# Optimization experiments

Measured on AMD Instinct MI355X. Metric: run time of the kernel, lower is better.

## Reference

```python
import jax, jax.numpy as jnp
import numpy as np

N_NODES = 100000
N_EDGES = 3200000
D_IN = 128
D_HID = 16
N_CLS = 2


def gcn_conv(x, edge_index, W, b, n_nodes):
    """PyG GCNConv (normalize=True, add_self_loops=True, bias=True)."""
    h = x @ W  # [N, out]
    loop = jnp.arange(n_nodes, dtype=edge_index.dtype)
    src = jnp.concatenate([edge_index[0], loop])
    dst = jnp.concatenate([edge_index[1], loop])
    deg = jax.ops.segment_sum(jnp.ones_like(dst, dtype=h.dtype), dst, num_segments=n_nodes)
    dinv = jnp.where(deg > 0, jax.lax.rsqrt(deg), jnp.zeros_like(deg))
    norm = dinv[src] * dinv[dst]  # [E+N]
    msg = h[src] * norm[:, None]  # gather + scale
    out = jax.ops.segment_sum(msg, dst, num_segments=n_nodes)  # scatter-add
    return out + b


def setup_inputs() -> dict:
    key = jax.random.key(0)
    k1, k2, k3, k4, k5 = jax.random.split(key, 5)
    x = jax.random.normal(k1, (N_NODES, D_IN), dtype=jnp.float32)
    edge_index = jax.random.randint(k2, (2, N_EDGES), 0, N_NODES, dtype=jnp.int64)
    # Glorot-style init for GCNConv weights, zeros for bias (PyG default)
    W1 = jax.random.normal(k3, (D_IN, D_HID), dtype=jnp.float32) * (1.0 / np.sqrt(D_IN))
    b1 = jnp.zeros((D_HID,), dtype=jnp.float32)
    W2 = jax.random.normal(k4, (D_HID, N_CLS), dtype=jnp.float32) * (1.0 / np.sqrt(D_HID))
    b2 = jnp.zeros((N_CLS,), dtype=jnp.float32)
    return {"x": x, "edge_index": edge_index, "W1": W1, "b1": b1, "W2": W2, "b2": b2}


def reference(x, edge_index, W1, b1, W2, b2):
    n = x.shape[0]
    h = gcn_conv(x, edge_index, W1, b1, n)
    h = jax.nn.relu(h)
    # dropout is identity in eval mode
    h = gcn_conv(h, edge_index, W2, b2, n)
    return jax.nn.log_softmax(h, axis=1)
```

## Files before the change

kernel.cpp:

```cpp
#include <hip/hip_runtime.h>
#include <hip/hip_bf16.h>
#include <hip/hip_fp16.h>

#define D_IN  128
#define D_HID 16
#define N_CLS 2
#define NPB   256
#define MAXB  512
#define TILE  8192
#define FPSCALE 65536.0f
#define FPINV   (1.0f / 65536.0f)

#define FE 0

__global__ void k_detect(const int* __restrict__ ev, int* __restrict__ flags) {
    __shared__ int sE;
    if (threadIdx.x == 0) sE = 0;
    __syncthreads();
    if (ev[2 * threadIdx.x + 1] != 0) atomicOr(&sE, 1);
    __syncthreads();
    if (threadIdx.x == 0) flags[FE] = sE ? 0 : 1;
}

template<bool I64>
__device__ __forceinline__ int lde(const void* p, size_t i) {
    if constexpr (I64) return (int)((const long long*)p)[i];
    else               return ((const int*)p)[i];
}

__global__ void k_bhist(const void* __restrict__ ei, unsigned int* __restrict__ gbcnt,
                        int E, const int* __restrict__ flags) {
    __shared__ unsigned int h[MAXB];
    for (int i = threadIdx.x; i < MAXB; i += blockDim.x) h[i] = 0u;
    __syncthreads();
    int stride = gridDim.x * blockDim.x;
    if (flags[FE]) {
        for (int e = blockIdx.x * blockDim.x + threadIdx.x; e < E; e += stride)
            atomicAdd(&h[lde<true>(ei, (size_t)E + e) >> 8], 1u);
    } else {
        for (int e = blockIdx.x * blockDim.x + threadIdx.x; e < E; e += stride)
            atomicAdd(&h[lde<false>(ei, (size_t)E + e) >> 8], 1u);
    }
    __syncthreads();
    for (int i = threadIdx.x; i < MAXB; i += blockDim.x)
        if (h[i]) atomicAdd(&gbcnt[i], h[i]);
}

__global__ void k_bscan(const unsigned int* __restrict__ gbcnt, int* __restrict__ bbase,
                        unsigned int* __restrict__ gcur, int nb) {
    __shared__ int s[MAXB];
    int tid = threadIdx.x;
    int v = (tid < nb) ? (int)gbcnt[tid] : 0;
    s[tid] = v;
    __syncthreads();
#pragma unroll
    for (int off = 1; off < MAXB; off <<= 1) {
        int t = (tid >= off) ? s[tid - off] : 0;
        __syncthreads();
        s[tid] += t;
        __syncthreads();
    }
    int excl = s[tid] - v;
    if (tid <= nb) bbase[tid] = (tid < nb) ? excl : s[nb - 1];
    if (tid < nb)  gcur[tid] = (unsigned int)excl;
}

template<bool I64>
__device__ __forceinline__ void part_body(
        const void* __restrict__ ei, unsigned int* __restrict__ gcur,
        unsigned int* __restrict__ staged, int E,
        unsigned int* sbuf, unsigned short* bbuf,
        int* hist, int* scn, int* lbase, int* gb) {
    int tid = threadIdx.x;
    int t0 = blockIdx.x * TILE;

    hist[tid] = 0;
    __syncthreads();

    int myB[16]; unsigned int myP[16]; int myR[16];
#pragma unroll
    for (int k = 0; k < 16; ++k) {
        int e = t0 + k * 512 + tid;
        if (e < E) {
            int s = lde<I64>(ei, (size_t)e);
            int d = lde<I64>(ei, (size_t)E + e);
            int b = d >> 8;
            myB[k] = b;
            myP[k] = ((unsigned int)s << 8) | (unsigned int)(d & 255);
            myR[k] = atomicAdd(&hist[b], 1);
        } else myB[k] = -1;
    }
    __syncthreads();

    int v = hist[tid];
    scn[tid] = v;
    __syncthreads();
#pragma unroll
    for (int off = 1; off < MAXB; off <<= 1) {
        int t = (tid >= off) ? scn[tid - off] : 0;
        __syncthreads();
        scn[tid] += t;
        __syncthreads();
    }
    int excl = scn[tid] - v;
    lbase[tid] = excl;
    int gb_ = 0;
    if (v > 0) gb_ = (int)atomicAdd(&gcur[tid], (unsigned int)v);
    gb[tid] = gb_;
    __syncthreads();

#pragma unroll
    for (int k = 0; k < 16; ++k) {
        if (myB[k] >= 0) {
            int pos = lbase[myB[k]] + myR[k];
            sbuf[pos] = myP[k];
            bbuf[pos] = (unsigned short)myB[k];
        }
    }
    __syncthreads();

    int tot = scn[MAXB - 1];
    for (int i = tid; i < tot; i += 512) {
        int b = bbuf[i];
        staged[(size_t)gb[b] + (i - lbase[b])] = sbuf[i];
    }
}

__global__ __launch_bounds__(512) void k_part(
        const void* __restrict__ ei, unsigned int* __restrict__ gcur,
        unsigned int* __restrict__ staged, int E, const int* __restrict__ flags) {
    __shared__ unsigned int sbuf[TILE];
    __shared__ unsigned short bbuf[TILE];
    __shared__ int hist[MAXB], scn[MAXB], lbase[MAXB], gb[MAXB];
    if (flags[FE]) part_body<true >(ei, gcur, staged, E, sbuf, bbuf, hist, scn, lbase, gb);
    else           part_body<false>(ei, gcur, staged, E, sbuf, bbuf, hist, scn, lbase, gb);
}

__global__ __launch_bounds__(512) void k_dinv2(
        const unsigned int* __restrict__ staged, const int* __restrict__ bbase,
        float* __restrict__ dinv, int N) {
    __shared__ unsigned int h[NPB];
    int tid = threadIdx.x, b = blockIdx.x;
    int s0 = bbase[b], cnt = bbase[b + 1] - s0;
    if (tid < NPB) h[tid] = 0u;
    __syncthreads();
    for (int j0 = tid * 8; j0 < cnt; j0 += 4096) {
        int jm = cnt - j0; if (jm > 8) jm = 8;
        unsigned int p[8];
#pragma unroll
        for (int i = 0; i < 8; ++i) if (i < jm) p[i] = staged[(size_t)s0 + j0 + i];
#pragma unroll
        for (int i = 0; i < 8; ++i) if (i < jm) atomicAdd(&h[p[i] & 255], 1u);
    }
    __syncthreads();
    int base = b * NPB, nn = N - base; if (nn > NPB) nn = NPB;
    if (tid < nn) dinv[base + tid] = rsqrtf((float)(h[tid] + 1u));
}

__global__ __launch_bounds__(256) void k_gemm1x(
        const float* __restrict__ x, const float* __restrict__ W1,
        const float* __restrict__ dinv, __half* __restrict__ g1h, int n) {
    __shared__ float wT[16][132];
    int tid = threadIdx.x;
    for (int i = tid; i < D_IN * D_HID; i += 256) {
        int f = i >> 7, k = i & 127;
        wT[f][k] = W1[k * D_HID + f];
    }
    __syncthreads();
    int f = tid & 15, q = tid >> 4;
    int nb0 = blockIdx.x * 64 + q * 4;
    if (nb0 >= n) return;
    const float* wr = &wT[f][0];
    const float* xb = x + (size_t)nb0 * D_IN;
    float a0 = 0.f, a1 = 0.f, a2 = 0.f, a3 = 0.f;
    if (nb0 + 4 <= n) {
#pragma unroll 8
        for (int k4 = 0; k4 < 32; ++k4) {
            float4 w4 = *(const float4*)(wr + k4 * 4);
            float4 x0 = *(const float4*)(xb + 0 * D_IN + k4 * 4);
            float4 x1 = *(const float4*)(xb + 1 * D_IN + k4 * 4);
            float4 x2 = *(const float4*)(xb + 2 * D_IN + k4 * 4);
            float4 x3 = *(const float4*)(xb + 3 * D_IN + k4 * 4);
            a0 += x0.x * w4.x + x0.y * w4.y + x0.z * w4.z + x0.w * w4.w;
            a1 += x1.x * w4.x + x1.y * w4.y + x1.z * w4.z + x1.w * w4.w;
            a2 += x2.x * w4.x + x2.y * w4.y + x2.z * w4.z + x2.w * w4.w;
            a3 += x3.x * w4.x + x3.y * w4.y + x3.z * w4.z + x3.w * w4.w;
        }
        g1h[(size_t)(nb0 + 0) * D_HID + f] = __float2half(dinv[nb0 + 0] * a0);
        g1h[(size_t)(nb0 + 1) * D_HID + f] = __float2half(dinv[nb0 + 1] * a1);
        g1h[(size_t)(nb0 + 2) * D_HID + f] = __float2half(dinv[nb0 + 2] * a2);
        g1h[(size_t)(nb0 + 3) * D_HID + f] = __float2half(dinv[nb0 + 3] * a3);
    } else {
        int m = n - nb0;
        for (int k4 = 0; k4 < 32; ++k4) {
            float4 w4 = *(const float4*)(wr + k4 * 4);
            for (int j = 0; j < m; ++j) {
                float4 xv = *(const float4*)(xb + j * D_IN + k4 * 4);
                float s = xv.x * w4.x + xv.y * w4.y + xv.z * w4.z + xv.w * w4.w;
                if (j == 0) a0 += s; else if (j == 1) a1 += s; else a2 += s;
            }
        }
        for (int j = 0; j < m; ++j) {
            float aj = (j == 0) ? a0 : ((j == 1) ? a1 : a2);
            g1h[(size_t)(nb0 + j) * D_HID + f] = __float2half(dinv[nb0 + j] * aj);
        }
    }
}

__global__ __launch_bounds__(1024) void k_agg1b(
        const unsigned int* __restrict__ staged, const int* __restrict__ bbase,
        const __half* __restrict__ g1h, const float* __restrict__ dinv,
        const float* __restrict__ b1, const float* __restrict__ W2,
        float2* __restrict__ g2, int N) {
    __shared__ int accI[NPB * D_HID];
    int tid = threadIdx.x, b = blockIdx.x;
    int s0 = bbase[b], cnt = bbase[b + 1] - s0;
    int base = b * NPB;
    for (int i = tid; i < NPB * D_HID; i += 1024) accI[i] = 0;
    __syncthreads();
    const __half2* g1h2 = (const __half2*)g1h;
    int f2 = tid & 7;
    int eg = tid >> 3;
    for (int j0 = eg * 8; j0 < cnt; j0 += 1024) {
        int jm = cnt - j0; if (jm > 8) jm = 8;
        unsigned int p[8]; float2 v[8];
#pragma unroll
        for (int i = 0; i < 8; ++i) if (i < jm) p[i] = staged[(size_t)s0 + j0 + i];
#pragma unroll
        for (int i = 0; i < 8; ++i) if (i < jm)
            v[i] = __half22float2(g1h2[(size_t)(p[i] >> 8) * 8 + f2]);
#pragma unroll
        for (int i = 0; i < 8; ++i) if (i < jm) {
            int a = (int)(p[i] & 255) * D_HID + f2 * 2;
            atomicAdd(&accI[a + 0], __float2int_rn(v[i].x * FPSCALE));
            atomicAdd(&accI[a + 1], __float2int_rn(v[i].y * FPSCALE));
        }
    }
    __syncthreads();
    int f = tid & 15;
    int gid = tid >> 4;
    int nn = N - base; if (nn > NPB) nn = NPB;
    for (int n = gid; n < nn; n += 64) {
        int gn = base + n;
        float acc = (float)accI[n * D_HID + f] * FPINV
                  + __half2float(g1h[(size_t)gn * D_HID + f]);
        float di = dinv[gn];
        float r = fmaxf(b1[f] + di * acc, 0.f);
        float c0 = r * W2[f * N_CLS + 0];
        float c1 = r * W2[f * N_CLS + 1];
#pragma unroll
        for (int m = 8; m >= 1; m >>= 1) {
            c0 += __shfl_xor(c0, m, 64);
            c1 += __shfl_xor(c1, m, 64);
        }
        if (f == 0) g2[gn] = make_float2(di * c0, di * c1);
    }
}

__global__ __launch_bounds__(512) void k_agg2b(
        const unsigned int* __restrict__ staged, const int* __restrict__ bbase,
        const float2* __restrict__ g2, const float* __restrict__ dinv,
        const float* __restrict__ b2, float2* __restrict__ out, int N) {
    __shared__ int accI[NPB * 2];
    int tid = threadIdx.x, b = blockIdx.x;
    int s0 = bbase[b], cnt = bbase[b + 1] - s0;
    int base = b * NPB;
    for (int i = tid; i < NPB * 2; i += 512) accI[i] = 0;
    __syncthreads();
    for (int j0 = tid * 4; j0 < cnt; j0 += 2048) {
        int jm = cnt - j0; if (jm > 4) jm = 4;
        unsigned int p[4]; float2 t[4];
#pragma unroll
        for (int i = 0; i < 4; ++i) if (i < jm) p[i] = staged[(size_t)s0 + j0 + i];
#pragma unroll
        for (int i = 0; i < 4; ++i) if (i < jm) t[i] = g2[p[i] >> 8];
#pragma unroll
        for (int i = 0; i < 4; ++i) if (i < jm) {
            int dl = (int)(p[i] & 255);
            atomicAdd(&accI[dl * 2 + 0], __float2int_rn(t[i].x * FPSCALE));
            atomicAdd(&accI[dl * 2 + 1], __float2int_rn(t[i].y * FPSCALE));
        }
    }
    __syncthreads();
    int nn = N - base; if (nn > NPB) nn = NPB;
    for (int n = tid; n < nn; n += 512) {
        int gn = base + n;
        float2 self = g2[gn];
        float di = dinv[gn];
        float v0 = b2[0] + di * ((float)accI[n * 2 + 0] * FPINV + self.x);
        float v1 = b2[1] + di * ((float)accI[n * 2 + 1] * FPINV + self.y);
        float mx = fmaxf(v0, v1);
        float lse = mx + logf(expf(v0 - mx) + expf(v1 - mx));
        out[gn] = make_float2(v0 - lse, v1 - lse);
    }
}

__global__ void fb_deg_init(unsigned int* __restrict__ deg, int n) {
    int i = blockIdx.x * blockDim.x + threadIdx.x;
    if (i < n) deg[i] = 1u;
}
template<bool I64>
__global__ void fb_deg_count(const void* __restrict__ ei, unsigned int* __restrict__ deg,
                             int E, const int* __restrict__ flags) {
    if (flags[FE] != (int)I64) return;
    int e = blockIdx.x * blockDim.x + threadIdx.x;
    if (e < E) atomicAdd(&deg[lde<I64>(ei, (size_t)E + e)], 1u);
}
__global__ void fb_dinv_inplace(float* __restrict__ dinv, int n) {
    int i = blockIdx.x * blockDim.x + threadIdx.x;
    if (i < n) {
        unsigned int u = ((const unsigned int*)dinv)[i];
        dinv[i] = rsqrtf((float)u);
    }
}
__global__ void fb_a1_init(const float* __restrict__ h1, const float* __restrict__ dinv,
                           const float* __restrict__ b1, float* __restrict__ a1, int n) {
    int tid = blockIdx.x * blockDim.x + threadIdx.x;
    if (tid >= n * D_HID) return;
    int node = tid >> 4, f = tid & 15;
    float di = dinv[node];
    a1[tid] = b1[f] + di * di * h1[tid];
}
template<bool I64>
__global__ void fb_agg1(const void* __restrict__ ei, const float* __restrict__ dinv,
                        const float* __restrict__ h1, float* __restrict__ a1,
                        int E, const int* __restrict__ flags) {
    if (flags[FE] != (int)I64) return;
    int tid = blockIdx.x * blockDim.x + threadIdx.x;
    int e = tid >> 4, f = tid & 15;
    if (e >= E) return;
    int s = lde<I64>(ei, (size_t)e);
    int d = lde<I64>(ei, (size_t)E + e);
    float norm = dinv[s] * dinv[d];
    atomicAdd(&a1[(size_t)d * D_HID + f], h1[(size_t)s * D_HID + f] * norm);
}
__global__ void fb_relu_gemm2(const float* __restrict__ a1, const float* __restrict__ W2,
                              float* __restrict__ h2, int n) {
    int node = blockIdx.x * blockDim.x + threadIdx.x;
    if (node >= n) return;
    float c0 = 0.f, c1 = 0.f;
    const float* row = a1 + (size_t)node * D_HID;
#pragma unroll
    for (int f = 0; f < D_HID; ++f) {
        float r = fmaxf(row[f], 0.f);
        c0 += r * W2[f * N_CLS + 0];
        c1 += r * W2[f * N_CLS + 1];
    }
    h2[(size_t)node * 2 + 0] = c0;
    h2[(size_t)node * 2 + 1] = c1;
}
__global__ void fb_a2_init(const float* __restrict__ h2, const float* __restrict__ dinv,
                           const float* __restrict__ b2, float* __restrict__ a2, int n) {
    int tid = blockIdx.x * blockDim.x + threadIdx.x;
    if (tid >= n * N_CLS) return;
    int node = tid >> 1, c = tid & 1;
    float di = dinv[node];
    a2[tid] = b2[c] + di * di * h2[tid];
}
template<bool I64>
__global__ void fb_agg2(const void* __restrict__ ei, const float* __restrict__ dinv,
                        const float* __restrict__ h2, float* __restrict__ a2,
                        int E, const int* __restrict__ flags) {
    if (flags[FE] != (int)I64) return;
    int e = blockIdx.x * blockDim.x + threadIdx.x;
    if (e >= E) return;
    int s = lde<I64>(ei, (size_t)e);
    int d = lde<I64>(ei, (size_t)E + e);
    float norm = dinv[s] * dinv[d];
    atomicAdd(&a2[(size_t)d * 2 + 0], h2[(size_t)s * 2 + 0] * norm);
    atomicAdd(&a2[(size_t)d * 2 + 1], h2[(size_t)s * 2 + 1] * norm);
}
__global__ void fb_gemm1(const float* __restrict__ x, const float* __restrict__ W1,
                         float* __restrict__ h1, int n) {
    __shared__ float w[D_IN * D_HID];
    for (int i = threadIdx.x; i < D_IN * D_HID; i += blockDim.x) w[i] = W1[i];
    __syncthreads();
    int tid = blockIdx.x * blockDim.x + threadIdx.x;
    int node = tid >> 4, f = tid & 15;
    if (node >= n) return;
    const float4* xr = (const float4*)(x + (size_t)node * D_IN);
    float acc = 0.f;
#pragma unroll
    for (int k4 = 0; k4 < D_IN / 4; ++k4) {
        float4 v = xr[k4];
        int k = k4 * 4;
        acc += v.x * w[(k + 0) * D_HID + f];
        acc += v.y * w[(k + 1) * D_HID + f];
        acc += v.z * w[(k + 2) * D_HID + f];
        acc += v.w * w[(k + 3) * D_HID + f];
    }
    h1[tid] = acc;
}
__global__ void fb_lsm(const float* __restrict__ a2, float* __restrict__ out, int n) {
    int node = blockIdx.x * blockDim.x + threadIdx.x;
    if (node >= n) return;
    float v0 = a2[(size_t)node * 2 + 0];
    float v1 = a2[(size_t)node * 2 + 1];
    float m = fmaxf(v0, v1);
    float lse = m + logf(expf(v0 - m) + expf(v1 - m));
    out[(size_t)node * 2 + 0] = v0 - lse;
    out[(size_t)node * 2 + 1] = v1 - lse;
}

extern "C" void kernel_launch(void* const* d_in, const int* in_sizes, int n_in,
                              void* d_out, int out_size, void* d_ws, size_t ws_size,
                              hipStream_t stream) {
    const float* x  = (const float*)d_in[0];
    const void*  ei = d_in[1];
    const float* W1 = (const float*)d_in[2];
    const float* b1 = (const float*)d_in[3];
    const float* W2 = (const float*)d_in[4];
    const float* b2 = (const float*)d_in[5];

    const int N = in_sizes[0] / D_IN;
    const int E = in_sizes[1] / 2;
    const int nb = (N + NPB - 1) / NPB;

    const int B = 256;
    dim3 blk(B);
    const int nBlkN = (N + B - 1) / B;
    const int nBlkE = (E + B - 1) / B;
    char* ws = (char*)d_ws;

    const size_t oDinv  = 0;
    const size_t oGBcnt = (size_t)N * 4;
    const size_t oBB    = oGBcnt + (size_t)nb * 4;
    const size_t oGcur  = oBB + (size_t)(nb + 1) * 4;
    const size_t oFlag  = oGcur + (size_t)nb * 4;
    const size_t oStage = (oFlag + 8 + 63) & ~(size_t)63;
    const size_t oG1h   = oStage + (size_t)E * 4;
    const size_t oG2    = oG1h + (size_t)N * D_HID * 2;
    const size_t needNew = oG2 + (size_t)N * 2 * 4;

    if (ws_size >= needNew && nb <= MAXB) {
        float*        dinv   = (float*)(ws + oDinv);
        unsigned int* gbcnt  = (unsigned int*)(ws + oGBcnt);
        int*          bbase  = (int*)(ws + oBB);
        unsigned int* gcur   = (unsigned int*)(ws + oGcur);
        int*          flags  = (int*)(ws + oFlag);
        unsigned int* staged = (unsigned int*)(ws + oStage);
        __half*       g1h    = (__half*)(ws + oG1h);
        float2*       g2     = (float2*)(ws + oG2);

        k_detect<<<dim3(1), blk, 0, stream>>>((const int*)ei, flags);
        hipMemsetAsync(gbcnt, 0, (size_t)nb * 4, stream);

        k_bhist<<<dim3(256), blk, 0, stream>>>(ei, gbcnt, E, flags);
        k_bscan<<<dim3(1), dim3(MAXB), 0, stream>>>(gbcnt, bbase, gcur, nb);

        dim3 gPart((E + TILE - 1) / TILE);
        k_part<<<gPart, dim3(512), 0, stream>>>(ei, gcur, staged, E, flags);

        k_dinv2<<<dim3(nb), dim3(512), 0, stream>>>(staged, bbase, dinv, N);

        k_gemm1x<<<dim3((N + 63) / 64), dim3(256), 0, stream>>>(x, W1, dinv, g1h, N);
        k_agg1b<<<dim3(nb), dim3(1024), 0, stream>>>(staged, bbase, g1h, dinv, b1, W2, g2, N);
        k_agg2b<<<dim3(nb), dim3(512), 0, stream>>>(staged, bbase, g2, dinv, b2,
                                                    (float2*)d_out, N);
    } else {
        float* dinv  = (float*)(ws + 0);
        float* h1    = (float*)(ws + 400128);
        float* a1    = (float*)(ws + 6800256);
        float* h2    = (float*)(ws + 13200384);
        float* a2    = (float*)(ws + 14000512);
        int*   flags = (int*)  (ws + 14800640);

        k_detect<<<dim3(1), blk, 0, stream>>>((const int*)ei, flags);
        fb_deg_init<<<dim3(nBlkN), blk, 0, stream>>>((unsigned int*)dinv, N);
        fb_deg_count<false><<<dim3(nBlkE), blk, 0, stream>>>(ei, (unsigned int*)dinv, E, flags);
        fb_deg_count<true ><<<dim3(nBlkE), blk, 0, stream>>>(ei, (unsigned int*)dinv, E, flags);
        fb_dinv_inplace<<<dim3(nBlkN), blk, 0, stream>>>(dinv, N);

        dim3 g_nh((N * D_HID + B - 1) / B);
        fb_gemm1<<<g_nh, blk, 0, stream>>>(x, W1, h1, N);
        fb_a1_init<<<g_nh, blk, 0, stream>>>(h1, dinv, b1, a1, N);
        dim3 g_eh(((size_t)E * D_HID + B - 1) / B);
        fb_agg1<false><<<g_eh, blk, 0, stream>>>(ei, dinv, h1, a1, E, flags);
        fb_agg1<true ><<<g_eh, blk, 0, stream>>>(ei, dinv, h1, a1, E, flags);
        fb_relu_gemm2<<<dim3(nBlkN), blk, 0, stream>>>(a1, W2, h2, N);
        dim3 g_n2((N * N_CLS + B - 1) / B);
        fb_a2_init<<<g_n2, blk, 0, stream>>>(h2, dinv, b2, a2, N);
        fb_agg2<false><<<dim3(nBlkE), blk, 0, stream>>>(ei, dinv, h2, a2, E, flags);
        fb_agg2<true ><<<dim3(nBlkE), blk, 0, stream>>>(ei, dinv, h2, a2, E, flags);
        fb_lsm<<<dim3(nBlkN), blk, 0, stream>>>(a2, (float*)d_out, N);
    }
}
```

Before: 238.5 us.

## Compute first-layer GEMM with split-bf16 MFMA instead of scalar FMA

Replaces the scalar fp32 x@W1 kernel with an MFMA version. x and W1 are split into hi/lo bf16 parts in shared memory, and three 16x16x32 bf16 MFMAs per K chunk approximate fp32 accuracy. The goal is to cut the ALU work of the dense projection and use coalesced float4 staging loads. It adds conversion work and extra shared memory, and precision is slightly lower than true fp32. The GEMM is one of several kernels and is probably bound by reading x (51 MB), so the overall gain may be small.

Measured after the change: 223.3 us. -6.4%, faster.

```diff
diff --git a/kernel.cpp b/kernel.cpp
--- a/kernel.cpp
+++ b/kernel.cpp
@@ -10,8 +10,18 @@
 #define TILE  8192
 #define FPSCALE 65536.0f
 #define FPINV   (1.0f / 65536.0f)
+#define XROW  136
 
 #define FE 0
+
+typedef short bf16x8 __attribute__((ext_vector_type(8)));
+typedef float f32x4  __attribute__((ext_vector_type(4)));
+
+__device__ __forceinline__ unsigned short f2bf(float f) {
+    unsigned int u = __float_as_uint(f);
+    u += 0x7FFFu + ((u >> 16) & 1u);
+    return (unsigned short)(u >> 16);
+}
 
 __global__ void k_detect(const int* __restrict__ ev, int* __restrict__ flags) {
     __shared__ int sE;
@@ -157,53 +167,66 @@
     if (tid < nn) dinv[base + tid] = rsqrtf((float)(h[tid] + 1u));
 }
 
-__global__ __launch_bounds__(256) void k_gemm1x(
+__global__ __launch_bounds__(256) void k_gemm1m(
         const float* __restrict__ x, const float* __restrict__ W1,
         const float* __restrict__ dinv, __half* __restrict__ g1h, int n) {
-    __shared__ float wT[16][132];
+    __shared__ short xhi[64 * XROW];
+    __shared__ short xlo[64 * XROW];
+    __shared__ short whi[16 * XROW];
+    __shared__ short wlo[16 * XROW];
     int tid = threadIdx.x;
+    int node0 = blockIdx.x * 64;
+
     for (int i = tid; i < D_IN * D_HID; i += 256) {
-        int f = i >> 7, k = i & 127;
-        wT[f][k] = W1[k * D_HID + f];
-    }
-    __syncthreads();
-    int f = tid & 15, q = tid >> 4;
-    int nb0 = blockIdx.x * 64 + q * 4;
-    if (nb0 >= n) return;
-    const float* wr = &wT[f][0];
-    const float* xb = x + (size_t)nb0 * D_IN;
-    float a0 = 0.f, a1 = 0.f, a2 = 0.f, a3 = 0.f;
-    if (nb0 + 4 <= n) {
-#pragma unroll 8
-        for (int k4 = 0; k4 < 32; ++k4) {
-            float4 w4 = *(const float4*)(wr + k4 * 4);
-            float4 x0 = *(const float4*)(xb + 0 * D_IN + k4 * 4);
-            float4 x1 = *(const float4*)(xb + 1 * D_IN + k4 * 4);
-            float4 x2 = *(const float4*)(xb + 2 * D_IN + k4 * 4);
-            float4 x3 = *(const float4*)(xb + 3 * D_IN + k4 * 4);
-            a0 += x0.x * w4.x + x0.y * w4.y + x0.z * w4.z + x0.w * w4.w;
-            a1 += x1.x * w4.x + x1.y * w4.y + x1.z * w4.z + x1.w * w4.w;
-            a2 += x2.x * w4.x + x2.y * w4.y + x2.z * w4.z + x2.w * w4.w;
-            a3 += x3.x * w4.x + x3.y * w4.y + x3.z * w4.z + x3.w * w4.w;
-        }
-        g1h[(size_t)(nb0 + 0) * D_HID + f] = __float2half(dinv[nb0 + 0] * a0);
-        g1h[(size_t)(nb0 + 1) * D_HID + f] = __float2half(dinv[nb0 + 1] * a1);
-        g1h[(size_t)(nb0 + 2) * D_HID + f] = __float2half(dinv[nb0 + 2] * a2);
-        g1h[(size_t)(nb0 + 3) * D_HID + f] = __float2half(dinv[nb0 + 3] * a3);
-    } else {
-        int m = n - nb0;
-        for (int k4 = 0; k4 < 32; ++k4) {
-            float4 w4 = *(const float4*)(wr + k4 * 4);
-            for (int j = 0; j < m; ++j) {
-                float4 xv = *(const float4*)(xb + j * D_IN + k4 * 4);
-                float s = xv.x * w4.x + xv.y * w4.y + xv.z * w4.z + xv.w * w4.w;
-                if (j == 0) a0 += s; else if (j == 1) a1 += s; else a2 += s;
-            }
-        }
-        for (int j = 0; j < m; ++j) {
-            float aj = (j == 0) ? a0 : ((j == 1) ? a1 : a2);
-            g1h[(size_t)(nb0 + j) * D_HID + f] = __float2half(dinv[nb0 + j] * aj);
-        }
+        int k = i >> 4, f = i & 15;
+        float v = W1[i];
+        unsigned short h = f2bf(v);
+        float fh = __uint_as_float(((unsigned int)h) << 16);
+        whi[f * XROW + k] = (short)h;
+        wlo[f * XROW + k] = (short)f2bf(v - fh);
+    }
+    int limFlat = (n - node0) * D_IN;
+#pragma unroll
+    for (int it = 0; it < 8; ++it) {
+        int flat = it * 1024 + tid * 4;
+        float4 v = make_float4(0.f, 0.f, 0.f, 0.f);
+        if (flat < limFlat) v = *(const float4*)(x + (size_t)node0 * D_IN + flat);
+        int row = flat >> 7, k = flat & 127;
+        unsigned short h0 = f2bf(v.x), h1 = f2bf(v.y), h2 = f2bf(v.z), h3 = f2bf(v.w);
+        unsigned short l0 = f2bf(v.x - __uint_as_float(((unsigned int)h0) << 16));
+        unsigned short l1 = f2bf(v.y - __uint_as_float(((unsigned int)h1) << 16));
+        unsigned short l2 = f2bf(v.z - __uint_as_float(((unsigned int)h2) << 16));
+        unsigned short l3 = f2bf(v.w - __uint_as_float(((unsigned int)h3) << 16));
+        int o = row * XROW + k;
+        *(uint2*)(&xhi[o]) = make_uint2((unsigned int)h0 | ((unsigned int)h1 << 16),
+                                        (unsigned int)h2 | ((unsigned int)h3 << 16));
+        *(uint2*)(&xlo[o]) = make_uint2((unsigned int)l0 | ((unsigned int)l1 << 16),
+                                        (unsigned int)l2 | ((unsigned int)l3 << 16));
+    }
+    __syncthreads();
+
+    int w = tid >> 6, L = tid & 63;
+    int m = L & 15, q = L >> 4;
+    const short* axh = &xhi[(w * 16 + m) * XROW + q * 8];
+    const short* axl = &xlo[(w * 16 + m) * XROW + q * 8];
+    const short* bwh = &whi[m * XROW + q * 8];
+    const short* bwl = &wlo[m * XROW + q * 8];
+    f32x4 acc = {0.f, 0.f, 0.f, 0.f};
+#pragma unroll
+    for (int c = 0; c < 4; ++c) {
+        bf16x8 ah = *(const bf16x8*)(axh + c * 32);
+        bf16x8 al = *(const bf16x8*)(axl + c * 32);
+        bf16x8 bh = *(const bf16x8*)(bwh + c * 32);
+        bf16x8 bl = *(const bf16x8*)(bwl + c * 32);
+        acc = __builtin_amdgcn_mfma_f32_16x16x32_bf16(ah, bh, acc, 0, 0, 0);
+        acc = __builtin_amdgcn_mfma_f32_16x16x32_bf16(ah, bl, acc, 0, 0, 0);
+        acc = __builtin_amdgcn_mfma_f32_16x16x32_bf16(al, bh, acc, 0, 0, 0);
+    }
+    int nodeB = node0 + w * 16 + q * 4;
+#pragma unroll
+    for (int r = 0; r < 4; ++r) {
+        int node = nodeB + r;
+        if (node < n) g1h[(size_t)node * D_HID + m] = __float2half(dinv[node] * acc[r]);
     }
 }
 
@@ -453,7 +476,7 @@
 
         k_dinv2<<<dim3(nb), dim3(512), 0, stream>>>(staged, bbase, dinv, N);
 
-        k_gemm1x<<<dim3((N + 63) / 64), dim3(256), 0, stream>>>(x, W1, dinv, g1h, N);
+        k_gemm1m<<<dim3((N + 63) / 64), dim3(256), 0, stream>>>(x, W1, dinv, g1h, N);
         k_agg1b<<<dim3(nb), dim3(1024), 0, stream>>>(staged, bbase, g1h, dinv, b1, W2, g2, N);
         k_agg2b<<<dim3(nb), dim3(512), 0, stream>>>(staged, bbase, g2, dinv, b2,
                                                     (float2*)d_out, N);
```
